# Kernel optimization log

Hardware: AMD Instinct MI355X
Metric: run time of the kernel (lower is better)

Reference implementation:

```python
import jax, jax.numpy as jnp
import numpy as np


def setup_inputs() -> dict:
    key = jax.random.key(0)
    k0, k1, k2, k3 = jax.random.split(key, 4)
    B, S, D, F, E = 2, 2048, 1024, 4096, 8
    hidden_states = jax.random.normal(k0, (B, S, D), dtype=jnp.float32)
    Wr = jax.random.normal(k1, (E, D), dtype=jnp.float32) * 0.02   # router Linear weight [E, D]
    W1 = jax.random.normal(k2, (E, D, F), dtype=jnp.float32) * 0.02  # expert w1 (transposed torch layout)
    W2 = jax.random.normal(k3, (E, F, D), dtype=jnp.float32) * 0.02  # expert w2
    return {"hidden_states": hidden_states, "Wr": Wr, "W1": W1, "W2": W2, "top_k": 2}


def reference(hidden_states, Wr, W1, W2, top_k):
    # hidden_states: [B, S, D]; Wr: [E, D]; W1: [E, D, F]; W2: [E, F, D]
    E = Wr.shape[0]
    dt = hidden_states.dtype

    # Router: logits -> top-k expert indices. NOTE: the original module computes
    # softmax routing weights over the top-k logits but never applies them in the
    # combine step, so the output is an UNWEIGHTED sum over selected experts.
    router_logits = jnp.einsum('bsd,ed->bse', hidden_states, Wr)
    _, topk_idx = jax.lax.top_k(router_logits, top_k)            # [B, S, K]

    # mask[b,s,e] = 1 if expert e is in token (b,s)'s top-k (indices are distinct)
    mask = (jax.nn.one_hot(topk_idx, E, dtype=dt).sum(axis=-2) > 0).astype(dt)  # [B, S, E]

    # Dense per-expert FFN (SiLU MLP, no bias, dropout=identity in eval):
    h = jax.nn.silu(jnp.einsum('bsd,edf->bsef', hidden_states, W1))  # [B, S, E, F]
    y = jnp.einsum('bsef,efd->bsed', h, W2)                          # [B, S, E, D]

    # Combine: unweighted sum over selected experts (faithful to source)
    return jnp.einsum('bsed,bse->bsd', y, mask)
```

## Files before the change

### kernel.cpp

```cpp
#include <hip/hip_runtime.h>
#include <hip/hip_bf16.h>
#include <stdint.h>

#define TOKENS 4096
#define DDIM 1024
#define FDIM 4096
#define NEXP 8
#define BM 256
#define BN 128
#define BK2 32

typedef __attribute__((ext_vector_type(4))) float f32x4;
typedef __attribute__((ext_vector_type(8))) short short8;

__device__ __forceinline__ unsigned short f2bf(float f) {
    union { float f; uint32_t u; } v; v.f = f;
    uint32_t u = v.u;
    return (unsigned short)((u + 0x7fff + ((u >> 16) & 1)) >> 16);
}

#define BARRIER() asm volatile("s_barrier" ::: "memory")
#define WAIT_VM0() asm volatile("s_waitcnt vmcnt(0)" ::: "memory")
#define WAIT_VM3() asm volatile("s_waitcnt vmcnt(3)" ::: "memory")
#define WAIT_LGKM0() asm volatile("s_waitcnt lgkmcnt(0)" ::: "memory")
#define GLDS(SRC, DST) __builtin_amdgcn_global_load_lds( \
    (const __attribute__((address_space(1))) void*)(SRC), \
    (__attribute__((address_space(3))) void*)(DST), 16, 0, 0)

__device__ __forceinline__ short8 dsr(uint32_t addr) {
    short8 d;
    asm volatile("ds_read_b128 %0, %1" : "=v"(d) : "v"(addr));
    return d;
}

__global__ __launch_bounds__(256) void cvt_x(const float* __restrict__ x,
                                             unsigned short* __restrict__ xb, int n) {
    int i = (blockIdx.x * 256 + threadIdx.x) * 8;
    if (i >= n) return;
    float4 a = *(const float4*)(x + i);
    float4 b = *(const float4*)(x + i + 4);
    short8 o;
    o[0] = f2bf(a.x); o[1] = f2bf(a.y); o[2] = f2bf(a.z); o[3] = f2bf(a.w);
    o[4] = f2bf(b.x); o[5] = f2bf(b.y); o[6] = f2bf(b.z); o[7] = f2bf(b.w);
    *(short8*)(xb + i) = o;
}

__global__ __launch_bounds__(256) void transpose_cvt(const float* __restrict__ in,
                                                     unsigned short* __restrict__ out,
                                                     int R, int C) {
    __shared__ float tile[32][33];
    int e = blockIdx.z;
    int r0 = blockIdx.y * 32, c0 = blockIdx.x * 32;
    const float* src = in + (size_t)e * R * C;
    unsigned short* dst = out + (size_t)e * R * C;
    int t = threadIdx.x;
    int rr = t >> 3;
    int cc = (t & 7) * 4;
    float4 v = *(const float4*)(src + (size_t)(r0 + rr) * C + c0 + cc);
    tile[rr][cc + 0] = v.x; tile[rr][cc + 1] = v.y;
    tile[rr][cc + 2] = v.z; tile[rr][cc + 3] = v.w;
    __syncthreads();
    int oc = rr;
    int orr = cc;
    ushort4 o;
    o.x = f2bf(tile[orr + 0][oc]);
    o.y = f2bf(tile[orr + 1][oc]);
    o.z = f2bf(tile[orr + 2][oc]);
    o.w = f2bf(tile[orr + 3][oc]);
    *(ushort4*)(dst + (size_t)(c0 + oc) * R + r0 + orr) = o;
}

__global__ __launch_bounds__(256) void router(const float* __restrict__ x,
                                              const float* __restrict__ wr,
                                              int* __restrict__ cnt,
                                              int* __restrict__ list) {
    __shared__ float wl[NEXP * DDIM];
    int t = threadIdx.x;
    for (int i = t; i < NEXP * DDIM; i += 256) wl[i] = wr[i];
    __syncthreads();
    int tok = blockIdx.x * 4 + (t >> 6);
    int lane = t & 63;
    float acc[NEXP];
#pragma unroll
    for (int e = 0; e < NEXP; e++) acc[e] = 0.f;
    const float* xr = x + (size_t)tok * DDIM;
    for (int d = lane; d < DDIM; d += 64) {
        float xv = xr[d];
#pragma unroll
        for (int e = 0; e < NEXP; e++) acc[e] += xv * wl[e * DDIM + d];
    }
#pragma unroll
    for (int e = 0; e < NEXP; e++) {
#pragma unroll
        for (int off = 32; off; off >>= 1) acc[e] += __shfl_xor(acc[e], off);
    }
    if (lane == 0) {
        int e1 = 0; float v1 = acc[0];
        for (int e = 1; e < NEXP; e++) if (acc[e] > v1) { v1 = acc[e]; e1 = e; }
        int e2 = -1; float v2 = -1e30f;
        for (int e = 0; e < NEXP; e++) if (e != e1 && acc[e] > v2) { v2 = acc[e]; e2 = e; }
        int p1 = atomicAdd(&cnt[e1], 1);
        list[e1 * TOKENS + p1] = tok;
        int p2 = atomicAdd(&cnt[e2], 1);
        list[e2 * TOKENS + p2] = tok;
    }
}

__global__ void setup(const int* __restrict__ cnt, int* __restrict__ off,
                      int* __restrict__ wbA, int* __restrict__ wbB,
                      int* __restrict__ qctr) {
    if (threadIdx.x == 0) {
        int s = 0, ta = 0, tb = 0;
        for (int e = 0; e < NEXP; e++) {
            off[e] = s; s += cnt[e];
            wbA[e] = ta; wbB[e] = tb;
            int ntm = (cnt[e] + BM - 1) >> 8;
            ta += ntm * (FDIM / BN);
            tb += ntm * (DDIM / BN) * 2;
        }
        wbA[NEXP] = ta; wbB[NEXP] = tb;
        qctr[0] = 0; qctr[1] = 0;
    }
}

template <bool GATHER_A, bool SILU, int KSPLIT>
__global__ __launch_bounds__(512, 2) void gemm_moe11(
    const unsigned short* __restrict__ Abase,
    const unsigned short* __restrict__ Wt,
    const int* __restrict__ cnt, const int* __restrict__ off,
    const int* __restrict__ list,
    const int* __restrict__ wbase,
    int* __restrict__ qctr,
    unsigned short* __restrict__ Hout,
    float* __restrict__ Yout,
    int KD, int KLEN, int NW) {
    __shared__ alignas(16) unsigned short As[3][BM * BK2];
    __shared__ alignas(16) unsigned short Bs[3][BN * BK2];
    __shared__ int wsh;

    const int t = threadIdx.x;
    const int lane = t & 63;
    const int wid = t >> 6;
    const int wm = wid >> 1, wn = wid & 1;
    const int r16 = lane & 15, g = lane >> 4;
    const int total = wbase[NEXP];

    const uint32_t asB = (uint32_t)(uintptr_t)&As[0][0];
    const uint32_t bsB = (uint32_t)(uintptr_t)&Bs[0][0];
    uint32_t aAdr[4], bAdr[4];
#pragma unroll
    for (int mi = 0; mi < 4; mi++) {
        int row = wm * 64 + mi * 16 + r16;
        aAdr[mi] = asB + row * 64 + ((g ^ ((row >> 1) & 3)) << 4);
    }
#pragma unroll
    for (int nj = 0; nj < 4; nj++) {
        int row = wn * 64 + nj * 16 + r16;
        bAdr[nj] = bsB + row * 64 + ((g ^ ((row >> 1) & 3)) << 4);
    }

    for (;;) {
        if (t == 0) wsh = atomicAdd(qctr, 1);
        __syncthreads();
        int w = wsh;
        if (w >= total) break;

        int e = 0;
        while (e < NEXP - 1 && w >= wbase[e + 1]) e++;
        w -= wbase[e];
        const int n_e = cnt[e];
        const int ntm = (n_e + BM - 1) >> 8;
        int combined = w / ntm;
        const int mtile = w - combined * ntm;
        const int kc = (KSPLIT == 2) ? (combined & 1) : 0;
        const int idx = (KSPLIT == 2) ? (combined >> 1) : combined;
        const int m0 = mtile * BM;
        const int n0 = idx * BN;
        const int base = off[e];
        const int k0 = kc * KLEN;

        const unsigned short* pA[2];
        int ldsA[2];
#pragma unroll
        for (int i = 0; i < 2; i++) {
            int c = i * 512 + t;
            int row = c >> 2, p = c & 3;
            int cg = p ^ ((row >> 1) & 3);
            int arow = m0 + row; if (arow >= n_e) arow = n_e - 1;
            size_t grow = GATHER_A ? (size_t)list[e * TOKENS + arow] : (size_t)(base + arow);
            pA[i] = Abase + grow * (size_t)KD + k0 + (cg << 3);
            ldsA[i] = c * 16;
        }
        const unsigned short* pB;
        int ldsB;
        {
            int c = t;
            int row = c >> 2, p = c & 3;
            int cg = p ^ ((row >> 1) & 3);
            pB = Wt + ((size_t)e * NW + n0 + row) * (size_t)KD + k0 + (cg << 3);
            ldsB = c * 16;
        }

        f32x4 acc[4][4];
#pragma unroll
        for (int i = 0; i < 4; i++)
#pragma unroll
            for (int j = 0; j < 4; j++) acc[i][j] = f32x4{0.f, 0.f, 0.f, 0.f};

#pragma unroll
        for (int s = 0; s < 2; ++s) {
#pragma unroll
            for (int i = 0; i < 2; i++) { GLDS(pA[i], (char*)As[s] + ldsA[i]); pA[i] += BK2; }
            GLDS(pB, (char*)Bs[s] + ldsB); pB += BK2;
        }
        WAIT_VM3();
        BARRIER();

        uint32_t uA0 = 0, uA1 = 16384, uA2 = 32768;
        uint32_t uB0 = 0, uB1 = 8192, uB2 = 16384;

        const int NT = KLEN / BK2;
        for (int tk = 0; tk < NT; ++tk) {
            if (tk + 2 < NT) {
#pragma unroll
                for (int i = 0; i < 2; i++) { GLDS(pA[i], (char*)As[0] + uA2 + ldsA[i]); pA[i] += BK2; }
                GLDS(pB, (char*)Bs[0] + uB2 + ldsB); pB += BK2;
            }

            short8 a0 = dsr(aAdr[0] + uA0);
            short8 a1 = dsr(aAdr[1] + uA0);
            short8 a2 = dsr(aAdr[2] + uA0);
            short8 a3 = dsr(aAdr[3] + uA0);
            short8 b0 = dsr(bAdr[0] + uB0);
            short8 b1 = dsr(bAdr[1] + uB0);
            short8 b2 = dsr(bAdr[2] + uB0);
            short8 b3 = dsr(bAdr[3] + uB0);
            WAIT_LGKM0();
            __builtin_amdgcn_sched_barrier(0);

            __builtin_amdgcn_s_setprio(1);
            acc[0][0] = __builtin_amdgcn_mfma_f32_16x16x32_bf16(a0, b0, acc[0][0], 0, 0, 0);
            acc[0][1] = __builtin_amdgcn_mfma_f32_16x16x32_bf16(a0, b1, acc[0][1], 0, 0, 0);
            acc[0][2] = __builtin_amdgcn_mfma_f32_16x16x32_bf16(a0, b2, acc[0][2], 0, 0, 0);
            acc[0][3] = __builtin_amdgcn_mfma_f32_16x16x32_bf16(a0, b3, acc[0][3], 0, 0, 0);
            acc[1][0] = __builtin_amdgcn_mfma_f32_16x16x32_bf16(a1, b0, acc[1][0], 0, 0, 0);
            acc[1][1] = __builtin_amdgcn_mfma_f32_16x16x32_bf16(a1, b1, acc[1][1], 0, 0, 0);
            acc[1][2] = __builtin_amdgcn_mfma_f32_16x16x32_bf16(a1, b2, acc[1][2], 0, 0, 0);
            acc[1][3] = __builtin_amdgcn_mfma_f32_16x16x32_bf16(a1, b3, acc[1][3], 0, 0, 0);
            acc[2][0] = __builtin_amdgcn_mfma_f32_16x16x32_bf16(a2, b0, acc[2][0], 0, 0, 0);
            acc[2][1] = __builtin_amdgcn_mfma_f32_16x16x32_bf16(a2, b1, acc[2][1], 0, 0, 0);
            acc[2][2] = __builtin_amdgcn_mfma_f32_16x16x32_bf16(a2, b2, acc[2][2], 0, 0, 0);
            acc[2][3] = __builtin_amdgcn_mfma_f32_16x16x32_bf16(a2, b3, acc[2][3], 0, 0, 0);
            acc[3][0] = __builtin_amdgcn_mfma_f32_16x16x32_bf16(a3, b0, acc[3][0], 0, 0, 0);
            acc[3][1] = __builtin_amdgcn_mfma_f32_16x16x32_bf16(a3, b1, acc[3][1], 0, 0, 0);
            acc[3][2] = __builtin_amdgcn_mfma_f32_16x16x32_bf16(a3, b2, acc[3][2], 0, 0, 0);
            acc[3][3] = __builtin_amdgcn_mfma_f32_16x16x32_bf16(a3, b3, acc[3][3], 0, 0, 0);
            __builtin_amdgcn_s_setprio(0);

            if (tk + 1 < NT) {
                if (tk + 2 < NT) WAIT_VM3();
                else             WAIT_VM0();
                BARRIER();
            }
            uint32_t ta_ = uA0; uA0 = uA1; uA1 = uA2; uA2 = ta_;
            uint32_t tb_ = uB0; uB0 = uB1; uB1 = uB2; uB2 = tb_;
        }

#pragma unroll
        for (int mi = 0; mi < 4; ++mi) {
#pragma unroll
            for (int nj = 0; nj < 4; ++nj) {
#pragma unroll
                for (int qq = 0; qq < 4; ++qq) {
                    int lr = wm * 64 + mi * 16 + g * 4 + qq;
                    if (m0 + lr < n_e) {
                        int col = n0 + wn * 64 + nj * 16 + r16;
                        float v = acc[mi][nj][qq];
                        if (SILU) {
                            v = v / (1.f + __expf(-v));
                            Hout[(size_t)(base + m0 + lr) * NW + col] = f2bf(v);
                        } else {
                            int tok = list[e * TOKENS + m0 + lr];
                            atomicAdd(&Yout[(size_t)tok * NW + col], v);
                        }
                    }
                }
            }
        }
    }
}

extern "C" void kernel_launch(void* const* d_in, const int* in_sizes, int n_in,
                              void* d_out, int out_size, void* d_ws, size_t ws_size,
                              hipStream_t stream) {
    const float* X  = (const float*)d_in[0];
    const float* Wr = (const float*)d_in[1];
    const float* W1 = (const float*)d_in[2];
    const float* W2 = (const float*)d_in[3];
    float* Y = (float*)d_out;

    char* ws = (char*)d_ws;
    int* cnt  = (int*)(ws + 0);
    int* off  = (int*)(ws + 64);
    int* wbA  = (int*)(ws + 128);
    int* wbB  = (int*)(ws + 192);
    int* qctr = (int*)(ws + 256);
    int* list = (int*)(ws + 1024);
    unsigned short* Xb = (unsigned short*)(ws + (1ull << 20));
    unsigned short* WT = (unsigned short*)(ws + (16ull << 20));
    unsigned short* H  = (unsigned short*)(ws + (80ull << 20));

    hipMemsetAsync(d_out, 0, (size_t)out_size * sizeof(float), stream);
    hipMemsetAsync(cnt, 0, 32, stream);

    cvt_x<<<TOKENS * DDIM / (256 * 8), 256, 0, stream>>>(X, Xb, TOKENS * DDIM);
    router<<<TOKENS / 4, 256, 0, stream>>>(X, Wr, cnt, list);
    setup<<<1, 64, 0, stream>>>(cnt, off, wbA, wbB, qctr);

    transpose_cvt<<<dim3(FDIM / 32, DDIM / 32, NEXP), 256, 0, stream>>>(W1, WT, DDIM, FDIM);
    gemm_moe11<true, true, 1><<<512, 512, 0, stream>>>(
        Xb, WT, cnt, off, list, wbA, qctr + 0, H, nullptr, DDIM, DDIM, FDIM);

    transpose_cvt<<<dim3(DDIM / 32, FDIM / 32, NEXP), 256, 0, stream>>>(W2, WT, FDIM, DDIM);
    gemm_moe11<false, false, 2><<<512, 512, 0, stream>>>(
        H, WT, cnt, off, list, wbB, qctr + 1, nullptr, Y, FDIM, FDIM / 2, DDIM);
}
```

Measured before the change: 498.3 us.

## Switch GEMMs to double-buffered LDS, raise occupancy, and split-K by four

Cuts the LDS ring from triple to double buffering and waits for all loads each iteration, shrinking LDS per block so more blocks fit per CU. Launch bounds rise to 6 blocks per CU and the persistent grids grow from 512 to 768 blocks. The second GEMM splits K four ways instead of two, which doubles its work items but also doubles the atomic adds into the fp32 output. In exchange the prefetch runs only one stage ahead, so memory latency is hidden less within each block, and the tighter register budget may cause spills.

```diff
diff --git a/kernel.cpp b/kernel.cpp
--- a/kernel.cpp
+++ b/kernel.cpp
@@ -21,7 +21,6 @@
 
 #define BARRIER() asm volatile("s_barrier" ::: "memory")
 #define WAIT_VM0() asm volatile("s_waitcnt vmcnt(0)" ::: "memory")
-#define WAIT_VM3() asm volatile("s_waitcnt vmcnt(3)" ::: "memory")
 #define WAIT_LGKM0() asm volatile("s_waitcnt lgkmcnt(0)" ::: "memory")
 #define GLDS(SRC, DST) __builtin_amdgcn_global_load_lds( \
     (const __attribute__((address_space(1))) void*)(SRC), \
@@ -116,7 +115,7 @@
             wbA[e] = ta; wbB[e] = tb;
             int ntm = (cnt[e] + BM - 1) >> 8;
             ta += ntm * (FDIM / BN);
-            tb += ntm * (DDIM / BN) * 2;
+            tb += ntm * (DDIM / BN) * 4;
         }
         wbA[NEXP] = ta; wbB[NEXP] = tb;
         qctr[0] = 0; qctr[1] = 0;
@@ -124,7 +123,7 @@
 }
 
 template <bool GATHER_A, bool SILU, int KSPLIT>
-__global__ __launch_bounds__(512, 2) void gemm_moe11(
+__global__ __launch_bounds__(512, 6) void gemm_moe12(
     const unsigned short* __restrict__ Abase,
     const unsigned short* __restrict__ Wt,
     const int* __restrict__ cnt, const int* __restrict__ off,
@@ -134,8 +133,8 @@
     unsigned short* __restrict__ Hout,
     float* __restrict__ Yout,
     int KD, int KLEN, int NW) {
-    __shared__ alignas(16) unsigned short As[3][BM * BK2];
-    __shared__ alignas(16) unsigned short Bs[3][BN * BK2];
+    __shared__ alignas(16) unsigned short As[2][BM * BK2];
+    __shared__ alignas(16) unsigned short Bs[2][BN * BK2];
     __shared__ int wsh;
 
     const int t = threadIdx.x;
@@ -172,8 +171,8 @@
         const int ntm = (n_e + BM - 1) >> 8;
         int combined = w / ntm;
         const int mtile = w - combined * ntm;
-        const int kc = (KSPLIT == 2) ? (combined & 1) : 0;
-        const int idx = (KSPLIT == 2) ? (combined >> 1) : combined;
+        const int kc = (KSPLIT > 1) ? (combined & (KSPLIT - 1)) : 0;
+        const int idx = (KSPLIT > 1) ? (combined / KSPLIT) : combined;
         const int m0 = mtile * BM;
         const int n0 = idx * BN;
         const int base = off[e];
@@ -208,33 +207,33 @@
             for (int j = 0; j < 4; j++) acc[i][j] = f32x4{0.f, 0.f, 0.f, 0.f};
 
 #pragma unroll
-        for (int s = 0; s < 2; ++s) {
-#pragma unroll
-            for (int i = 0; i < 2; i++) { GLDS(pA[i], (char*)As[s] + ldsA[i]); pA[i] += BK2; }
-            GLDS(pB, (char*)Bs[s] + ldsB); pB += BK2;
-        }
-        WAIT_VM3();
+        for (int i = 0; i < 2; i++) { GLDS(pA[i], (char*)As[0] + ldsA[i]); pA[i] += BK2; }
+        GLDS(pB, (char*)Bs[0] + ldsB); pB += BK2;
+        WAIT_VM0();
         BARRIER();
-
-        uint32_t uA0 = 0, uA1 = 16384, uA2 = 32768;
-        uint32_t uB0 = 0, uB1 = 8192, uB2 = 16384;
 
         const int NT = KLEN / BK2;
         for (int tk = 0; tk < NT; ++tk) {
-            if (tk + 2 < NT) {
-#pragma unroll
-                for (int i = 0; i < 2; i++) { GLDS(pA[i], (char*)As[0] + uA2 + ldsA[i]); pA[i] += BK2; }
-                GLDS(pB, (char*)Bs[0] + uB2 + ldsB); pB += BK2;
+            const int cur = tk & 1;
+            const uint32_t oA = cur ? 16384u : 0u;
+            const uint32_t oB = cur ? 8192u : 0u;
+
+            if (tk + 1 < NT) {
+                char* Ad = (char*)As[cur ^ 1];
+                char* Bd = (char*)Bs[cur ^ 1];
+#pragma unroll
+                for (int i = 0; i < 2; i++) { GLDS(pA[i], Ad + ldsA[i]); pA[i] += BK2; }
+                GLDS(pB, Bd + ldsB); pB += BK2;
             }
 
-            short8 a0 = dsr(aAdr[0] + uA0);
-            short8 a1 = dsr(aAdr[1] + uA0);
-            short8 a2 = dsr(aAdr[2] + uA0);
-            short8 a3 = dsr(aAdr[3] + uA0);
-            short8 b0 = dsr(bAdr[0] + uB0);
-            short8 b1 = dsr(bAdr[1] + uB0);
-            short8 b2 = dsr(bAdr[2] + uB0);
-            short8 b3 = dsr(bAdr[3] + uB0);
+            short8 a0 = dsr(aAdr[0] + oA);
+            short8 a1 = dsr(aAdr[1] + oA);
+            short8 a2 = dsr(aAdr[2] + oA);
+            short8 a3 = dsr(aAdr[3] + oA);
+            short8 b0 = dsr(bAdr[0] + oB);
+            short8 b1 = dsr(bAdr[1] + oB);
+            short8 b2 = dsr(bAdr[2] + oB);
+            short8 b3 = dsr(bAdr[3] + oB);
             WAIT_LGKM0();
             __builtin_amdgcn_sched_barrier(0);
 
@@ -258,12 +257,9 @@
             __builtin_amdgcn_s_setprio(0);
 
             if (tk + 1 < NT) {
-                if (tk + 2 < NT) WAIT_VM3();
-                else             WAIT_VM0();
+                WAIT_VM0();
                 BARRIER();
             }
-            uint32_t ta_ = uA0; uA0 = uA1; uA1 = uA2; uA2 = ta_;
-            uint32_t tb_ = uB0; uB0 = uB1; uB1 = uB2; uB2 = tb_;
         }
 
 #pragma unroll
@@ -318,10 +314,10 @@
     setup<<<1, 64, 0, stream>>>(cnt, off, wbA, wbB, qctr);
 
     transpose_cvt<<<dim3(FDIM / 32, DDIM / 32, NEXP), 256, 0, stream>>>(W1, WT, DDIM, FDIM);
-    gemm_moe11<true, true, 1><<<512, 512, 0, stream>>>(
+    gemm_moe12<true, true, 1><<<768, 512, 0, stream>>>(
         Xb, WT, cnt, off, list, wbA, qctr + 0, H, nullptr, DDIM, DDIM, FDIM);
 
     transpose_cvt<<<dim3(DDIM / 32, FDIM / 32, NEXP), 256, 0, stream>>>(W2, WT, FDIM, DDIM);
-    gemm_moe11<false, false, 2><<<512, 512, 0, stream>>>(
-        H, WT, cnt, off, list, wbB, qctr + 1, nullptr, Y, FDIM, FDIM / 2, DDIM);
-}
+    gemm_moe12<false, false, 4><<<768, 512, 0, stream>>>(
+        H, WT, cnt, off, list, wbB, qctr + 1, nullptr, Y, FDIM, FDIM / 4, DDIM);
+}
```

New measurement: 1.952 ms. 292% more time.
